# Kernel optimization log

Hardware: AMD Instinct MI355X
Metric: run time of the kernel (lower is better)

The kernel has to match this reference:

```python
import jax, jax.numpy as jnp
import numpy as np
import math

N_POLY = 300
N_DEG = 3
OUT_DIM = 2 * (N_DEG + 1)  # 8 sampled points per query
HEADS = 8


def _grid_sample(x, grid):
    # x: [B,C,H,W], grid: [B,Q,N,2] in [-1,1]; bilinear, zeros padding, align_corners=False
    B, C, H, W = x.shape
    ix = (grid[..., 0] + 1.0) * (W * 0.5) - 0.5
    iy = (grid[..., 1] + 1.0) * (H * 0.5) - 0.5
    ix0 = jnp.floor(ix)
    iy0 = jnp.floor(iy)
    wx1 = ix - ix0
    wy1 = iy - iy0
    x0 = ix0.astype(jnp.int32)
    y0 = iy0.astype(jnp.int32)
    xf = x.reshape(B, C, H * W)

    def gather(yc, xc):
        valid = (xc >= 0) & (xc < W) & (yc >= 0) & (yc < H)
        idx = jnp.clip(yc, 0, H - 1) * W + jnp.clip(xc, 0, W - 1)  # [B,Q,N]
        vals = jax.vmap(lambda m, i: m[:, i])(xf, idx)  # [B,C,Q,N]
        return vals * valid[:, None].astype(x.dtype)

    out = (gather(y0, x0) * ((1 - wy1) * (1 - wx1))[:, None]
           + gather(y0, x0 + 1) * ((1 - wy1) * wx1)[:, None]
           + gather(y0 + 1, x0) * (wy1 * (1 - wx1))[:, None]
           + gather(y0 + 1, x0 + 1) * (wy1 * wx1)[:, None])
    return out  # [B,C,Q,N]


def setup_inputs() -> dict:
    key = jax.random.key(0)
    B, C, H, W = 16, 256, 64, 96
    ks = list(jax.random.split(key, 20))

    def w(k, shape):
        return jax.random.normal(k, shape, jnp.float32) * (1.0 / np.sqrt(shape[0]))

    d = {}
    d['x'] = jax.random.normal(ks[0], (B, C, H, W), jnp.float32)
    d['qs_w1'] = w(ks[1], (C, 2 * C)); d['qs_b1'] = jnp.zeros((2 * C,), jnp.float32)
    d['qs_w2'] = w(ks[2], (2 * C, 1)); d['qs_b2'] = jnp.zeros((1,), jnp.float32)
    d['rp_w1'] = w(ks[3], (C, 2 * C)); d['rp_b1'] = jnp.zeros((2 * C,), jnp.float32)
    d['rp_w2'] = w(ks[4], (2 * C, OUT_DIM * 2)); d['rp_b2'] = jnp.zeros((OUT_DIM * 2,), jnp.float32)
    d['mha_in_w'] = w(ks[5], (C, 3 * C)); d['mha_in_b'] = jnp.zeros((3 * C,), jnp.float32)
    d['mha_out_w'] = w(ks[6], (C, C)); d['mha_out_b'] = jnp.zeros((C,), jnp.float32)
    d['dq_w'] = w(ks[7], (C, C)); d['dq_b'] = jnp.zeros((C,), jnp.float32)
    d['dk_w'] = w(ks[8], (C, C)); d['dk_b'] = jnp.zeros((C,), jnp.float32)
    d['dv_w'] = w(ks[9], (C, C)); d['dv_b'] = jnp.zeros((C,), jnp.float32)
    d['ln1_g'] = jnp.ones((C,), jnp.float32); d['ln1_b'] = jnp.zeros((C,), jnp.float32)
    d['cl_w1'] = w(ks[10], (C, 2 * C)); d['cl_b1'] = jnp.zeros((2 * C,), jnp.float32)
    d['cl_w2'] = w(ks[11], (2 * C, 1)); d['cl_b2'] = jnp.zeros((1,), jnp.float32)
    d['po_w1'] = w(ks[12], (C, 2 * C)); d['po_b1'] = jnp.zeros((2 * C,), jnp.float32)
    d['po_w2'] = w(ks[13], (2 * C, OUT_DIM)); d['po_b2'] = jnp.zeros((OUT_DIM,), jnp.float32)
    return d


def reference(x, qs_w1, qs_b1, qs_w2, qs_b2, rp_w1, rp_b1, rp_w2, rp_b2,
              mha_in_w, mha_in_b, mha_out_w, mha_out_b,
              dq_w, dq_b, dk_w, dk_b, dv_w, dv_b,
              ln1_g, ln1_b, cl_w1, cl_b1, cl_w2, cl_b2,
              po_w1, po_b1, po_w2, po_b2):
    B, C, H, W = x.shape
    dh = C // HEADS
    scale = 1.0 / math.sqrt(dh)

    memory = x.reshape(B, C, H * W).transpose(0, 2, 1)  # [B,HW,C]
    logits = jax.nn.elu(memory @ qs_w1 + qs_b1) @ qs_w2 + qs_b2  # [B,HW,1]
    _, idxs = jax.lax.top_k(logits[..., 0], N_POLY)  # [B,Q]
    querys = jnp.take_along_axis(memory, idxs[..., None], axis=1)  # [B,Q,C]
    rp = jnp.tanh((memory @ rp_w1 + rp_b1) @ rp_w2 + rp_b2)  # [B,HW,2*OUT_DIM]
    ref = jnp.take_along_axis(rp, idxs[..., None], axis=1).reshape(B, N_POLY, OUT_DIM, 2)

    # self-attention (nn.MultiheadAttention, batch_first, 8 heads)
    qkv = querys @ mha_in_w + mha_in_b
    q, k, v = jnp.split(qkv, 3, axis=-1)
    sh = lambda t: t.reshape(B, N_POLY, HEADS, dh).transpose(0, 2, 1, 3)
    q, k, v = sh(q), sh(k), sh(v)
    att = jax.nn.softmax(jnp.einsum('bhqd,bhkd->bhqk', q, k) * scale, axis=-1)
    o = jnp.einsum('bhqk,bhkd->bhqd', att, v).transpose(0, 2, 1, 3).reshape(B, N_POLY, C)
    o = o @ mha_out_w + mha_out_b
    tgt = querys + o  # dropout is identity in eval
    mu = tgt.mean(-1, keepdims=True)
    var = tgt.var(-1, keepdims=True)
    tgt = (tgt - mu) / jnp.sqrt(var + 1e-5) * ln1_g + ln1_b

    # deformable attention
    dq = (tgt @ dq_w + dq_b).reshape(B, N_POLY, 1, HEADS, dh).transpose(0, 1, 3, 2, 4)  # [B,Q,H,1,dh]
    samp = _grid_sample(x, ref)  # [B,C,Q,N]
    sp = samp.transpose(0, 3, 2, 1)  # [B,N,Q,C] (matches torch transpose(1,-1))
    # faithful to torch .view(B,Q,N,H,dh) on the [B,N,Q,C] contiguous tensor: plain reshape
    dk = (sp @ dk_w + dk_b).reshape(B, N_POLY, OUT_DIM, HEADS, dh).transpose(0, 1, 3, 2, 4)  # [B,Q,H,N,dh]
    dv = (sp @ dv_w + dv_b).reshape(B, N_POLY, OUT_DIM, HEADS, dh).transpose(0, 1, 3, 2, 4)
    a = jax.nn.softmax(jnp.einsum('bqhod,bqhnd->bqhon', dq, dk) * scale, axis=-1)
    out2 = jnp.einsum('bqhon,bqhnd->bqhod', a, dv).reshape(B, N_POLY, C)
    tgt = tgt + out2

    poly = jax.nn.silu(tgt @ po_w1 + po_b1) @ po_w2 + po_b2
    cls = jax.nn.sigmoid(jax.nn.elu(tgt @ cl_w1 + cl_b1) @ cl_w2 + cl_b2)[..., 0]
    return poly.reshape(B, N_POLY, 2, N_DEG + 1), cls
```

## Files before the change

kernel.cpp:

```cpp
#include <hip/hip_runtime.h>
#include <hip/hip_bf16.h>
#include <math.h>

typedef __hip_bfloat16 bf16;

#define B_   16
#define C_   256
#define H_   64
#define W_   96
#define HW_  6144
#define Q_   300
#define NH_  8
#define DH_  32
#define HID_ 512
#define QB_  4
#define SCALE_ 0.17677669529663687f

__device__ __forceinline__ float b2f(bf16 v){ return __bfloat162float(v); }
__device__ __forceinline__ bf16 f2b(float v){ return __float2bfloat16(v); }
__device__ __forceinline__ int clampi(int v, int lo, int hi){
  return v < lo ? lo : (v > hi ? hi : v);
}

__global__ __launch_bounds__(256) void xt_k(const float* __restrict__ x,
                                            float* __restrict__ xt){
  int b  = blockIdx.z;
  int c0 = blockIdx.y*64;
  int p0 = blockIdx.x*64;
  __shared__ float t[64][65];
  int tid = threadIdx.x;
  int tr = tid >> 6;
  int tc = tid & 63;
  #pragma unroll
  for (int i=0;i<16;i++){
    int cc = tr + i*4;
    t[cc][tc] = x[((size_t)b*C_ + c0+cc)*HW_ + p0 + tc];
  }
  __syncthreads();
  #pragma unroll
  for (int i=0;i<16;i++){
    int pp = tr + i*4;
    xt[((size_t)b*HW_ + p0+pp)*C_ + c0 + tc] = t[tc][pp];
  }
}

__global__ __launch_bounds__(256) void score_k(const float* __restrict__ x,
    const float* __restrict__ w1, const float* __restrict__ b1,
    const float* __restrict__ w2, const float* __restrict__ b2,
    float* __restrict__ logits){
  int b = blockIdx.y, hw0 = blockIdx.x*64;
  int tid = threadIdx.x;
  int tc = tid & 31;
  int tr = tid >> 5;
  __shared__ float xs[32][68];
  __shared__ float wsl[32][256];
  float (*red)[33] = (float(*)[33])wsl;
  float part[8];
  #pragma unroll
  for (int i=0;i<8;i++) part[i]=0.f;
  for (int pass=0; pass<2; ++pass){
    float acc[8][8];
    #pragma unroll
    for (int i=0;i<8;i++)
      #pragma unroll
      for (int j=0;j<8;j++) acc[i][j]=0.f;
    for (int kt=0; kt<8; ++kt){
      #pragma unroll
      for (int i=0;i<2;i++){
        int e = tid + i*256;
        int rr4 = e & 15, kk = e >> 4;
        *reinterpret_cast<float4*>(&xs[kk][rr4*4]) =
          *reinterpret_cast<const float4*>(&x[(size_t)(b*C_ + kt*32+kk)*HW_ + hw0 + rr4*4]);
      }
      #pragma unroll
      for (int i=0;i<8;i++){
        int e = tid + i*256;
        int jj4 = e & 63, kk = e >> 6;
        *reinterpret_cast<float4*>(&wsl[kk][jj4*4]) =
          *reinterpret_cast<const float4*>(&w1[(size_t)(kt*32+kk)*HID_ + pass*256 + jj4*4]);
      }
      __syncthreads();
      #pragma unroll
      for (int k=0;k<32;k++){
        float4 a0 = *reinterpret_cast<float4*>(&xs[k][tr*8]);
        float4 a1 = *reinterpret_cast<float4*>(&xs[k][tr*8+4]);
        float4 w0 = *reinterpret_cast<float4*>(&wsl[k][tc*4]);
        float4 w4 = *reinterpret_cast<float4*>(&wsl[k][128 + tc*4]);
        float aa[8] = {a0.x,a0.y,a0.z,a0.w,a1.x,a1.y,a1.z,a1.w};
        float ww[8] = {w0.x,w0.y,w0.z,w0.w,w4.x,w4.y,w4.z,w4.w};
        #pragma unroll
        for (int i=0;i<8;i++)
          #pragma unroll
          for (int j=0;j<8;j++)
            acc[i][j] += aa[i]*ww[j];
      }
      __syncthreads();
    }
    #pragma unroll
    for (int j=0;j<8;j++){
      int col = (j < 4) ? (tc*4 + j) : (128 + tc*4 + (j-4));
      int jg = pass*256 + col;
      float bb = b1[jg], w2v = w2[jg];
      #pragma unroll
      for (int i=0;i<8;i++){
        float h = acc[i][j] + bb;
        h = h > 0.f ? h : expm1f(h);
        part[i] += h * w2v;
      }
    }
  }
  #pragma unroll
  for (int i=0;i<8;i++) red[tr*8+i][tc] = part[i];
  __syncthreads();
  if (tid < 64){
    float s = 0.f;
    for (int t=0;t<32;t++) s += red[tid][t];
    logits[(size_t)b*HW_ + hw0 + tid] = s + b2[0];
  }
}

__global__ __launch_bounds__(1024) void topk_k(const float* __restrict__ logits,
                                               int* __restrict__ idxs){
  int b = blockIdx.x, tid = threadIdx.x;
  __shared__ unsigned long long keys[8192];
  for (int i = tid; i < 8192; i += 1024){
    unsigned long long key = 0ull;
    if (i < HW_){
      float v = logits[(size_t)b*HW_ + i];
      unsigned u = __float_as_uint(v);
      unsigned m = (u & 0x80000000u) ? ~u : (u ^ 0x80000000u);
      if (!(v == v)) m = 0u;
      key = ((unsigned long long)m << 32) | (unsigned)(HW_ - 1 - i);
    }
    keys[i] = key;
  }
  __syncthreads();
  for (int k = 2; k <= 8192; k <<= 1){
    for (int j = k >> 1; j >= 1; j >>= 1){
      for (int i = tid; i < 8192; i += 1024){
        int l = i ^ j;
        if (l > i){
          unsigned long long a = keys[i], c = keys[l];
          bool sw = ((i & k) == 0) ? (a < c) : (a > c);
          if (sw){ keys[i] = c; keys[l] = a; }
        }
      }
      __syncthreads();
    }
  }
  if (tid < Q_){
    int idx = HW_ - 1 - (int)(keys[tid] & 0xFFFFFFFFull);
    idxs[b*Q_ + tid] = idx;
  }
}

template<int XT>
__global__ __launch_bounds__(256) void qproj_k(const float* __restrict__ x,
    const float* __restrict__ xt,
    const int* __restrict__ idxs,
    const float* __restrict__ rw1, const float* __restrict__ rb1,
    const float* __restrict__ rw2, const float* __restrict__ rb2,
    const float* __restrict__ mw,  const float* __restrict__ mb,
    float* __restrict__ refs,
    bf16* __restrict__ qarr, bf16* __restrict__ karr, bf16* __restrict__ varr){
  int blk = blockIdx.x;
  int b = blk/(Q_/QB_), q0 = (blk%(Q_/QB_))*QB_;
  int tid = threadIdx.x;
  __shared__ float rowl[QB_][C_];
  __shared__ float hl[QB_][HID_];
  __shared__ float red[16][17];
  int idxv[QB_];
  #pragma unroll
  for (int j=0;j<QB_;j++) idxv[j] = clampi(idxs[b*Q_+q0+j], 0, HW_-1);
  #pragma unroll
  for (int j=0;j<QB_;j++){
    if (XT) rowl[j][tid] = xt[((size_t)b*HW_ + idxv[j])*C_ + tid];
    else    rowl[j][tid] = x[((size_t)b*C_ + tid)*HW_ + idxv[j]];
  }
  __syncthreads();
  float h0[QB_], h1[QB_];
  #pragma unroll
  for (int j=0;j<QB_;j++){ h0[j]=rb1[tid]; h1[j]=rb1[tid+256]; }
  for (int c=0;c<C_;c++){
    float wv0 = rw1[(size_t)c*HID_ + tid];
    float wv1 = rw1[(size_t)c*HID_ + tid + 256];
    #pragma unroll
    for (int j=0;j<QB_;j++){
      float rv = rowl[j][c];
      h0[j] += rv*wv0; h1[j] += rv*wv1;
    }
  }
  #pragma unroll
  for (int j=0;j<QB_;j++){ hl[j][tid]=h0[j]; hl[j][tid+256]=h1[j]; }
  float aq[QB_], ak[QB_], av[QB_];
  #pragma unroll
  for (int j=0;j<QB_;j++){ aq[j]=mb[tid]; ak[j]=mb[tid+256]; av[j]=mb[tid+512]; }
  for (int c=0;c<C_;c++){
    const float* wr = mw + (size_t)c*768;
    float w0 = wr[tid], w1v = wr[tid+256], w2v = wr[tid+512];
    #pragma unroll
    for (int j=0;j<QB_;j++){
      float rv = rowl[j][c];
      aq[j] += rv*w0; ak[j] += rv*w1v; av[j] += rv*w2v;
    }
  }
  int h = tid>>5, d = tid&31;
  #pragma unroll
  for (int j=0;j<QB_;j++){
    size_t o = (((size_t)b*NH_+h)*Q_+(q0+j))*DH_ + d;
    qarr[o]=f2b(aq[j]); karr[o]=f2b(ak[j]); varr[o]=f2b(av[j]);
  }
  __syncthreads();
  int o = tid & 15, seg = tid >> 4;
  for (int j=0;j<QB_;j++){
    float p = 0.f;
    for (int jj=seg*32; jj<seg*32+32; jj++) p += hl[j][jj]*rw2[jj*16+o];
    red[seg][o] = p;
    __syncthreads();
    if (tid < 16){
      float s = 0.f;
      for (int sg=0; sg<16; sg++) s += red[sg][tid];
      refs[((size_t)b*Q_+(q0+j))*16 + tid] = tanhf(s + rb2[tid]);
    }
    __syncthreads();
  }
}

__global__ __launch_bounds__(256) void attn_k(const bf16* __restrict__ qarr,
    const bf16* __restrict__ karr, const bf16* __restrict__ varr,
    bf16* __restrict__ att_o){
  int blk = blockIdx.x; int bh = blk >> 1, half = blk & 1;
  int tid = threadIdx.x, rg = tid >> 5, lane = tid & 31;
  __shared__ bf16 kk[Q_][34];
  __shared__ bf16 vv[Q_][34];
  __shared__ float ps[8][304];
  __shared__ float qsl[8][32];
  const bf16* kb = karr + (size_t)bh*Q_*DH_;
  const bf16* vb = varr + (size_t)bh*Q_*DH_;
  const bf16* qb = qarr + (size_t)bh*Q_*DH_;
  for (int e=tid; e<Q_*DH_; e+=256){
    int k = e >> 5, d = e & 31;
    kk[k][d] = kb[e];
    vv[k][d] = vb[e];
  }
  __syncthreads();
  int b = bh >> 3, h = bh & 7;
  int rbase = half*150;
  for (int p0=0; p0<150; p0+=8){
    int rr = p0 + rg;
    bool act = rr < 150;
    int r = rbase + (act ? rr : 0);
    float qd = act ? b2f(qb[r*DH_ + lane]) : 0.f;
    qsl[rg][lane] = qd;
    __syncthreads();
    float lmax = -1e30f;
    for (int k=lane; k<Q_; k+=32){
      float s = 0.f;
      #pragma unroll
      for (int d=0; d<DH_; d++) s += qsl[rg][d]*b2f(kk[k][d]);
      s *= SCALE_;
      ps[rg][k] = s;
      lmax = fmaxf(lmax, s);
    }
    #pragma unroll
    for (int off=16; off>=1; off>>=1) lmax = fmaxf(lmax, __shfl_xor(lmax, off, 32));
    float lsum = 0.f;
    for (int k=lane; k<Q_; k+=32){
      float e = expf(ps[rg][k] - lmax);
      ps[rg][k] = e;
      lsum += e;
    }
    #pragma unroll
    for (int off=16; off>=1; off>>=1) lsum += __shfl_xor(lsum, off, 32);
    __syncthreads();
    float out = 0.f;
    for (int k=0;k<Q_;k++) out += ps[rg][k]*b2f(vv[k][lane]);
    if (act) att_o[((size_t)b*Q_ + r)*C_ + h*DH_ + lane] = f2b(out / lsum);
    __syncthreads();
  }
}

template<int XT>
__global__ __launch_bounds__(256) void proj_ln_k(const bf16* __restrict__ att_o,
    const float* __restrict__ x, const float* __restrict__ xt,
    const int* __restrict__ idxs,
    const float* __restrict__ ow, const float* __restrict__ ob,
    const float* __restrict__ g,  const float* __restrict__ beta,
    const float* __restrict__ dqw, const float* __restrict__ dqb,
    float* __restrict__ tgt, float* __restrict__ dqv){
  int blk = blockIdx.x, tid = threadIdx.x;
  int b = blk/Q_, qq = blk%Q_;
  __shared__ float ol[C_];
  __shared__ float yl[C_];
  __shared__ float rs[4], rs2[4];
  size_t base = (size_t)blk*C_;
  ol[tid] = b2f(att_o[base+tid]);
  __syncthreads();
  float acc = ob[tid];
  for (int c=0;c<C_;c++) acc += ol[c]*ow[(size_t)c*C_+tid];
  int idx = clampi(idxs[b*Q_+qq], 0, HW_-1);
  float resid;
  if (XT) resid = xt[((size_t)b*HW_ + idx)*C_ + tid];
  else    resid = x[((size_t)b*C_ + tid)*HW_ + idx];
  float t = resid + acc;
  float s = t, s2 = t*t;
  #pragma unroll
  for (int off=32; off>=1; off>>=1){
    s  += __shfl_xor(s,  off, 64);
    s2 += __shfl_xor(s2, off, 64);
  }
  if ((tid&63)==0){ rs[tid>>6]=s; rs2[tid>>6]=s2; }
  __syncthreads();
  float ts=0.f, ts2=0.f;
  #pragma unroll
  for (int w=0;w<4;w++){ ts+=rs[w]; ts2+=rs2[w]; }
  float mu = ts*(1.f/256.f);
  float var = ts2*(1.f/256.f) - mu*mu;
  if (!(var > 0.f)) var = 0.f;
  float y = (t-mu)*rsqrtf(var+1e-5f)*g[tid] + beta[tid];
  tgt[base+tid] = y;
  yl[tid] = y;
  __syncthreads();
  float a2 = dqb[tid];
  for (int c=0;c<C_;c++) a2 += yl[c]*dqw[(size_t)c*C_+tid];
  dqv[base+tid] = a2;
}

template<int XT>
__global__ __launch_bounds__(512) void deform_k(const float* __restrict__ x,
    const float* __restrict__ xt,
    const float* __restrict__ refs, const float* __restrict__ dqv,
    const float* __restrict__ tgt,
    const float* __restrict__ dkw, const float* __restrict__ dkb,
    const float* __restrict__ dvw, const float* __restrict__ dvb,
    const float* __restrict__ pw1, const float* __restrict__ pb1,
    const float* __restrict__ pw2, const float* __restrict__ pb2,
    const float* __restrict__ cw1, const float* __restrict__ cb1,
    const float* __restrict__ cw2, const float* __restrict__ cb2,
    float* __restrict__ out_poly, float* __restrict__ out_cls){
  int blk = blockIdx.x; int b = blk/(Q_/QB_), qg = blk%(Q_/QB_);
  int q0 = qg*QB_;
  int tid = threadIdx.x;
  int col = tid & 255;
  int half = tid >> 8;
  __shared__ float smem_u[32*C_];
  float (*rows_l)[C_]  = (float(*)[C_])smem_u;
  float (*hp)[HID_]    = (float(*)[HID_])smem_u;
  float (*hc)[HID_]    = (float(*)[HID_])(smem_u + QB_*HID_);
  __shared__ float tl[QB_][C_];
  __shared__ float grefs[32][2];
  __shared__ float redp[16][8];
  __shared__ float redc[16];
  if (tid < 64){
    int rloc = tid >> 1, comp = tid & 1;
    int r = qg*32 + rloc;
    int n = r/Q_, q = r - n*Q_;
    grefs[rloc][comp] = refs[(((size_t)b*Q_+q)*8+n)*2 + comp];
  }
  __syncthreads();
  const float* xc  = x  + ((size_t)b*C_ + col)*HW_;
  const float* xbt = xt + (size_t)b*HW_*C_;
  for (int i=0; i<16; ++i){
    int rloc = half*16 + i;
    float gx = grefs[rloc][0];
    float gy = grefs[rloc][1];
    if (!(gx > -2.f && gx < 2.f)) gx = 0.f;
    if (!(gy > -2.f && gy < 2.f)) gy = 0.f;
    float ix = (gx + 1.f)*48.f - 0.5f;
    float iy = (gy + 1.f)*32.f - 0.5f;
    float fx = floorf(ix), fy = floorf(iy);
    int x0 = (int)fx, y0 = (int)fy;
    float wx1 = ix - fx, wy1 = iy - fy;
    float wx0 = 1.f - wx1, wy0 = 1.f - wy1;
    float v = 0.f;
    if (XT){
      if (y0   >= 0 && y0   < H_ && x0   >= 0 && x0   < W_) v += wy0*wx0*xbt[(size_t)(y0*W_+x0)*C_ + col];
      if (y0   >= 0 && y0   < H_ && x0+1 >= 0 && x0+1 < W_) v += wy0*wx1*xbt[(size_t)(y0*W_+x0+1)*C_ + col];
      if (y0+1 >= 0 && y0+1 < H_ && x0   >= 0 && x0   < W_) v += wy1*wx0*xbt[(size_t)((y0+1)*W_+x0)*C_ + col];
      if (y0+1 >= 0 && y0+1 < H_ && x0+1 >= 0 && x0+1 < W_) v += wy1*wx1*xbt[(size_t)((y0+1)*W_+x0+1)*C_ + col];
    } else {
      if (y0   >= 0 && y0   < H_ && x0   >= 0 && x0   < W_) v += wy0*wx0*xc[y0*W_+x0];
      if (y0   >= 0 && y0   < H_ && x0+1 >= 0 && x0+1 < W_) v += wy0*wx1*xc[y0*W_+x0+1];
      if (y0+1 >= 0 && y0+1 < H_ && x0   >= 0 && x0   < W_) v += wy1*wx0*xc[(y0+1)*W_+x0];
      if (y0+1 >= 0 && y0+1 < H_ && x0+1 >= 0 && x0+1 < W_) v += wy1*wx1*xc[(y0+1)*W_+x0+1];
    }
    rows_l[rloc][col] = v;
  }
  __syncthreads();
  float ka[16], va[16];
  float kbb = dkb[col], vbb = dvb[col];
  #pragma unroll
  for (int rr=0; rr<16; ++rr){ ka[rr]=kbb; va[rr]=vbb; }
  for (int c=0; c<C_; c+=4){
    float wk0 = dkw[(size_t)(c+0)*C_+col], wk1 = dkw[(size_t)(c+1)*C_+col];
    float wk2 = dkw[(size_t)(c+2)*C_+col], wk3 = dkw[(size_t)(c+3)*C_+col];
    float wv0 = dvw[(size_t)(c+0)*C_+col], wv1 = dvw[(size_t)(c+1)*C_+col];
    float wv2 = dvw[(size_t)(c+2)*C_+col], wv3 = dvw[(size_t)(c+3)*C_+col];
    #pragma unroll
    for (int rr=0; rr<16; ++rr){
      float4 rv = *reinterpret_cast<float4*>(&rows_l[half*16+rr][c]);
      ka[rr] += rv.x*wk0 + rv.y*wk1 + rv.z*wk2 + rv.w*wk3;
      va[rr] += rv.x*wv0 + rv.y*wv1 + rv.z*wv2 + rv.w*wv3;
    }
  }
  #pragma unroll
  for (int jq=0; jq<2; ++jq){
    int jj = half*2 + jq;
    int q2 = q0 + jj;
    float qd = dqv[((size_t)b*Q_+q2)*C_ + col];
    float s[8];
    #pragma unroll
    for (int n=0;n<8;n++){
      float t_ = qd * ka[jq*8+n];
      #pragma unroll
      for (int off=16; off>=1; off>>=1) t_ += __shfl_xor(t_, off, 32);
      s[n] = t_ * SCALE_;
    }
    float m = s[0];
    #pragma unroll
    for (int n=1;n<8;n++) m = fmaxf(m, s[n]);
    float e[8], sum = 0.f;
    #pragma unroll
    for (int n=0;n<8;n++){ e[n] = expf(s[n]-m); sum += e[n]; }
    float inv = 1.f/sum;
    float out = 0.f;
    #pragma unroll
    for (int n=0;n<8;n++) out += e[n]*inv*va[jq*8+n];
    tl[jj][col] = tgt[((size_t)b*Q_+q2)*C_ + col] + out;
  }
  __syncthreads();
  float a[QB_], cc[QB_];
  #pragma unroll
  for (int jj=0;jj<QB_;jj++){ a[jj]=pb1[tid]; cc[jj]=cb1[tid]; }
  for (int c=0;c<C_;c++){
    float pwA = pw1[(size_t)c*HID_ + tid];
    float cwA = cw1[(size_t)c*HID_ + tid];
    #pragma unroll
    for (int jj=0;jj<QB_;jj++){
      float rv = tl[jj][c];
      a[jj] += rv*pwA; cc[jj] += rv*cwA;
    }
  }
  #pragma unroll
  for (int jj=0;jj<QB_;jj++){
    hp[jj][tid] = a[jj] * (1.f/(1.f+expf(-a[jj])));
    hc[jj][tid] = cc[jj] > 0.f ? cc[jj] : expm1f(cc[jj]);
  }
  __syncthreads();
  for (int jj=0;jj<QB_;jj++){
    if (tid < 128){
      int o = tid & 7, seg = tid >> 3;
      float p = 0.f;
      for (int j=seg*32; j<seg*32+32; j++) p += hp[jj][j]*pw2[j*8+o];
      redp[seg][o] = p;
    } else if (tid < 144){
      int seg = tid - 128;
      float p = 0.f;
      for (int j=seg*32; j<seg*32+32; j++) p += hc[jj][j]*cw2[j];
      redc[seg] = p;
    }
    __syncthreads();
    if (tid < 8){
      float sm = 0.f;
      for (int sg=0; sg<16; sg++) sm += redp[sg][tid];
      out_poly[((size_t)b*Q_+(q0+jj))*8 + tid] = sm + pb2[tid];
    }
    if (tid == 8){
      float sc = 0.f;
      for (int sg=0; sg<16; sg++) sc += redc[sg];
      sc += cb2[0];
      out_cls[b*Q_+(q0+jj)] = 1.f/(1.f+expf(-sc));
    }
    __syncthreads();
  }
}

extern "C" void kernel_launch(void* const* d_in, const int* in_sizes, int n_in,
                              void* d_out, int out_size, void* d_ws, size_t ws_size,
                              hipStream_t stream){
  (void)in_sizes; (void)out_size;
  if (n_in < 29) return;
  const float* x       = (const float*)d_in[0];
  const float* qs_w1   = (const float*)d_in[1];
  const float* qs_b1   = (const float*)d_in[2];
  const float* qs_w2   = (const float*)d_in[3];
  const float* qs_b2   = (const float*)d_in[4];
  const float* rp_w1   = (const float*)d_in[5];
  const float* rp_b1   = (const float*)d_in[6];
  const float* rp_w2   = (const float*)d_in[7];
  const float* rp_b2   = (const float*)d_in[8];
  const float* mha_in_w  = (const float*)d_in[9];
  const float* mha_in_b  = (const float*)d_in[10];
  const float* mha_out_w = (const float*)d_in[11];
  const float* mha_out_b = (const float*)d_in[12];
  const float* dq_w    = (const float*)d_in[13];
  const float* dq_b    = (const float*)d_in[14];
  const float* dk_w    = (const float*)d_in[15];
  const float* dk_b    = (const float*)d_in[16];
  const float* dv_w    = (const float*)d_in[17];
  const float* dv_b    = (const float*)d_in[18];
  const float* ln1_g   = (const float*)d_in[19];
  const float* ln1_b   = (const float*)d_in[20];
  const float* cl_w1   = (const float*)d_in[21];
  const float* cl_b1   = (const float*)d_in[22];
  const float* cl_w2   = (const float*)d_in[23];
  const float* cl_b2   = (const float*)d_in[24];
  const float* po_w1   = (const float*)d_in[25];
  const float* po_b1   = (const float*)d_in[26];
  const float* po_w2   = (const float*)d_in[27];
  const float* po_b2   = (const float*)d_in[28];

  constexpr size_t QKV1     = (size_t)B_*NH_*Q_*DH_;
  constexpr size_t SZ_R1    = 9830400;
  constexpr size_t OFF_IDXS = SZ_R1;
  constexpr size_t OFF_REFS = OFF_IDXS + 19200;
  constexpr size_t OFF_ATTO = OFF_REFS + 307200;
  constexpr size_t WS_NEED  = OFF_ATTO + 2457600;
  constexpr size_t OFF_XT   = WS_NEED;
  constexpr size_t SZ_XT    = (size_t)B_*HW_*C_*sizeof(float);
  constexpr size_t WS_NEED2 = OFF_XT + SZ_XT;
  if (ws_size < WS_NEED) return;
  const bool use_xt = (ws_size >= WS_NEED2);

  char* ws = (char*)d_ws;
  float* logits = (float*)(ws + 0);
  bf16*  qarr   = (bf16*) (ws + 0);
  bf16*  karr   = qarr + QKV1;
  bf16*  varr   = karr + QKV1;
  float* tgt    = (float*)(ws + 0);
  float* dqv    = (float*)(ws + 4915200);
  int*   idxs   = (int*)  (ws + OFF_IDXS);
  float* refs   = (float*)(ws + OFF_REFS);
  bf16*  att_o  = (bf16*) (ws + OFF_ATTO);
  float* xt     = (float*)(ws + OFF_XT);

  float* out_poly = (float*)d_out;
  float* out_cls  = out_poly + B_*Q_*8;

  if (use_xt)
    xt_k<<<dim3(HW_/64, C_/64, B_), 256, 0, stream>>>(x, xt);

  score_k<<<dim3(HW_/64, B_), 256, 0, stream>>>(x, qs_w1, qs_b1, qs_w2, qs_b2, logits);
  topk_k<<<B_, 1024, 0, stream>>>(logits, idxs);

  if (use_xt){
    qproj_k<1><<<B_*(Q_/QB_), 256, 0, stream>>>(x, xt, idxs, rp_w1, rp_b1, rp_w2, rp_b2,
                                                mha_in_w, mha_in_b, refs, qarr, karr, varr);
  } else {
    qproj_k<0><<<B_*(Q_/QB_), 256, 0, stream>>>(x, xt, idxs, rp_w1, rp_b1, rp_w2, rp_b2,
                                                mha_in_w, mha_in_b, refs, qarr, karr, varr);
  }
  attn_k<<<B_*NH_*2, 256, 0, stream>>>(qarr, karr, varr, att_o);
  if (use_xt){
    proj_ln_k<1><<<B_*Q_, 256, 0, stream>>>(att_o, x, xt, idxs, mha_out_w, mha_out_b,
                                            ln1_g, ln1_b, dq_w, dq_b, tgt, dqv);
    deform_k<1><<<B_*(Q_/QB_), 512, 0, stream>>>(x, xt, refs, dqv, tgt,
                                           dk_w, dk_b, dv_w, dv_b,
                                           po_w1, po_b1, po_w2, po_b2,
                                           cl_w1, cl_b1, cl_w2, cl_b2,
                                           out_poly, out_cls);
  } else {
    proj_ln_k<0><<<B_*Q_, 256, 0, stream>>>(att_o, x, xt, idxs, mha_out_w, mha_out_b,
                                            ln1_g, ln1_b, dq_w, dq_b, tgt, dqv);
    deform_k<0><<<B_*(Q_/QB_), 512, 0, stream>>>(x, xt, refs, dqv, tgt,
                                           dk_w, dk_b, dv_w, dv_b,
                                           po_w1, po_b1, po_w2, po_b2,
                                           cl_w1, cl_b1, cl_w2, cl_b2,
                                           out_poly, out_cls);
  }
}
```

Before: 1.274 ms.

## Raise queries per block in qproj and deform kernels to improve weight reuse

qproj_k now handles 6 queries per block instead of 4, so each weight load is reused across more rows. deform_k moves to 1024 threads covering 8 queries (64 sampled rows) per block, with a ceiling grid and tail guards, and splits the poly and cls MLP first layers across thread halves. The output reductions run for all queries in one pass rather than a per-query loop with syncs. The cost is a larger block, more shared memory and register pressure (launch_bounds 1024), and fewer blocks in the grid.

Measured after the change: 1.375 ms. +7.9%, slower.

```diff
diff --git a/kernel.cpp b/kernel.cpp
--- a/kernel.cpp
+++ b/kernel.cpp
@@ -14,6 +14,9 @@
 #define DH_  32
 #define HID_ 512
 #define QB_  4
+#define QPB_ 6
+#define QBD_ 8
+#define NQG_ ((Q_ + QBD_ - 1)/QBD_)
 #define SCALE_ 0.17677669529663687f
 
 __device__ __forceinline__ float b2f(bf16 v){ return __bfloat162float(v); }
@@ -164,55 +167,55 @@
     float* __restrict__ refs,
     bf16* __restrict__ qarr, bf16* __restrict__ karr, bf16* __restrict__ varr){
   int blk = blockIdx.x;
-  int b = blk/(Q_/QB_), q0 = (blk%(Q_/QB_))*QB_;
+  int b = blk/(Q_/QPB_), q0 = (blk%(Q_/QPB_))*QPB_;
   int tid = threadIdx.x;
-  __shared__ float rowl[QB_][C_];
-  __shared__ float hl[QB_][HID_];
+  __shared__ float rowl[QPB_][C_];
+  __shared__ float hl[QPB_][HID_];
   __shared__ float red[16][17];
-  int idxv[QB_];
-  #pragma unroll
-  for (int j=0;j<QB_;j++) idxv[j] = clampi(idxs[b*Q_+q0+j], 0, HW_-1);
-  #pragma unroll
-  for (int j=0;j<QB_;j++){
+  int idxv[QPB_];
+  #pragma unroll
+  for (int j=0;j<QPB_;j++) idxv[j] = clampi(idxs[b*Q_+q0+j], 0, HW_-1);
+  #pragma unroll
+  for (int j=0;j<QPB_;j++){
     if (XT) rowl[j][tid] = xt[((size_t)b*HW_ + idxv[j])*C_ + tid];
     else    rowl[j][tid] = x[((size_t)b*C_ + tid)*HW_ + idxv[j]];
   }
   __syncthreads();
-  float h0[QB_], h1[QB_];
-  #pragma unroll
-  for (int j=0;j<QB_;j++){ h0[j]=rb1[tid]; h1[j]=rb1[tid+256]; }
+  float h0[QPB_], h1[QPB_];
+  #pragma unroll
+  for (int j=0;j<QPB_;j++){ h0[j]=rb1[tid]; h1[j]=rb1[tid+256]; }
   for (int c=0;c<C_;c++){
     float wv0 = rw1[(size_t)c*HID_ + tid];
     float wv1 = rw1[(size_t)c*HID_ + tid + 256];
     #pragma unroll
-    for (int j=0;j<QB_;j++){
+    for (int j=0;j<QPB_;j++){
       float rv = rowl[j][c];
       h0[j] += rv*wv0; h1[j] += rv*wv1;
     }
   }
   #pragma unroll
-  for (int j=0;j<QB_;j++){ hl[j][tid]=h0[j]; hl[j][tid+256]=h1[j]; }
-  float aq[QB_], ak[QB_], av[QB_];
-  #pragma unroll
-  for (int j=0;j<QB_;j++){ aq[j]=mb[tid]; ak[j]=mb[tid+256]; av[j]=mb[tid+512]; }
+  for (int j=0;j<QPB_;j++){ hl[j][tid]=h0[j]; hl[j][tid+256]=h1[j]; }
+  float aq[QPB_], ak[QPB_], av[QPB_];
+  #pragma unroll
+  for (int j=0;j<QPB_;j++){ aq[j]=mb[tid]; ak[j]=mb[tid+256]; av[j]=mb[tid+512]; }
   for (int c=0;c<C_;c++){
     const float* wr = mw + (size_t)c*768;
     float w0 = wr[tid], w1v = wr[tid+256], w2v = wr[tid+512];
     #pragma unroll
-    for (int j=0;j<QB_;j++){
+    for (int j=0;j<QPB_;j++){
       float rv = rowl[j][c];
       aq[j] += rv*w0; ak[j] += rv*w1v; av[j] += rv*w2v;
     }
   }
   int h = tid>>5, d = tid&31;
   #pragma unroll
-  for (int j=0;j<QB_;j++){
+  for (int j=0;j<QPB_;j++){
     size_t o = (((size_t)b*NH_+h)*Q_+(q0+j))*DH_ + d;
     qarr[o]=f2b(aq[j]); karr[o]=f2b(ak[j]); varr[o]=f2b(av[j]);
   }
   __syncthreads();
   int o = tid & 15, seg = tid >> 4;
-  for (int j=0;j<QB_;j++){
+  for (int j=0;j<QPB_;j++){
     float p = 0.f;
     for (int jj=seg*32; jj<seg*32+32; jj++) p += hl[j][jj]*rw2[jj*16+o];
     red[seg][o] = p;
@@ -327,7 +330,7 @@
 }
 
 template<int XT>
-__global__ __launch_bounds__(512) void deform_k(const float* __restrict__ x,
+__global__ __launch_bounds__(1024, 8) void deform_k(const float* __restrict__ x,
     const float* __restrict__ xt,
     const float* __restrict__ refs, const float* __restrict__ dqv,
     const float* __restrict__ tgt,
@@ -338,30 +341,35 @@
     const float* __restrict__ cw1, const float* __restrict__ cb1,
     const float* __restrict__ cw2, const float* __restrict__ cb2,
     float* __restrict__ out_poly, float* __restrict__ out_cls){
-  int blk = blockIdx.x; int b = blk/(Q_/QB_), qg = blk%(Q_/QB_);
-  int q0 = qg*QB_;
+  int blk = blockIdx.x; int b = blk/NQG_, qg = blk%NQG_;
+  int q0 = qg*QBD_;
   int tid = threadIdx.x;
   int col = tid & 255;
-  int half = tid >> 8;
-  __shared__ float smem_u[32*C_];
-  float (*rows_l)[C_]  = (float(*)[C_])smem_u;
-  float (*hp)[HID_]    = (float(*)[HID_])smem_u;
-  float (*hc)[HID_]    = (float(*)[HID_])(smem_u + QB_*HID_);
-  __shared__ float tl[QB_][C_];
-  __shared__ float grefs[32][2];
-  __shared__ float redp[16][8];
-  __shared__ float redc[16];
-  if (tid < 64){
+  int quarter = tid >> 8;
+  __shared__ float smem_u[64*C_];
+  float (*rows_l)[C_] = (float(*)[C_])smem_u;
+  float (*hp)[HID_]   = (float(*)[HID_])smem_u;
+  float (*hc)[HID_]   = (float(*)[HID_])(smem_u + QBD_*HID_);
+  __shared__ float tl_u[QBD_*C_];
+  float (*tl)[C_]      = (float(*)[C_])tl_u;
+  float (*redp)[16][8] = (float(*)[16][8])tl_u;
+  float *redc          = tl_u + QBD_*16*8;
+  __shared__ float grefs[64][2];
+  if (tid < 128){
     int rloc = tid >> 1, comp = tid & 1;
-    int r = qg*32 + rloc;
-    int n = r/Q_, q = r - n*Q_;
-    grefs[rloc][comp] = refs[(((size_t)b*Q_+q)*8+n)*2 + comp];
+    int r = qg*64 + rloc;
+    float gv = 0.f;
+    if (r < Q_*8){
+      int n = r/Q_, q = r - n*Q_;
+      gv = refs[(((size_t)b*Q_+q)*8+n)*2 + comp];
+    }
+    grefs[rloc][comp] = gv;
   }
   __syncthreads();
   const float* xc  = x  + ((size_t)b*C_ + col)*HW_;
   const float* xbt = xt + (size_t)b*HW_*C_;
   for (int i=0; i<16; ++i){
-    int rloc = half*16 + i;
+    int rloc = quarter*16 + i;
     float gx = grefs[rloc][0];
     float gy = grefs[rloc][1];
     if (!(gx > -2.f && gx < 2.f)) gx = 0.f;
@@ -398,16 +406,17 @@
     float wv2 = dvw[(size_t)(c+2)*C_+col], wv3 = dvw[(size_t)(c+3)*C_+col];
     #pragma unroll
     for (int rr=0; rr<16; ++rr){
-      float4 rv = *reinterpret_cast<float4*>(&rows_l[half*16+rr][c]);
+      float4 rv = *reinterpret_cast<float4*>(&rows_l[quarter*16+rr][c]);
       ka[rr] += rv.x*wk0 + rv.y*wk1 + rv.z*wk2 + rv.w*wk3;
       va[rr] += rv.x*wv0 + rv.y*wv1 + rv.z*wv2 + rv.w*wv3;
     }
   }
   #pragma unroll
   for (int jq=0; jq<2; ++jq){
-    int jj = half*2 + jq;
+    int jj = quarter*2 + jq;
     int q2 = q0 + jj;
-    float qd = dqv[((size_t)b*Q_+q2)*C_ + col];
+    int q2c = q2 < Q_ ? q2 : Q_-1;
+    float qd = dqv[((size_t)b*Q_+q2c)*C_ + col];
     float s[8];
     #pragma unroll
     for (int n=0;n<8;n++){
@@ -426,52 +435,63 @@
     float out = 0.f;
     #pragma unroll
     for (int n=0;n<8;n++) out += e[n]*inv*va[jq*8+n];
-    tl[jj][col] = tgt[((size_t)b*Q_+q2)*C_ + col] + out;
-  }
-  __syncthreads();
-  float a[QB_], cc[QB_];
-  #pragma unroll
-  for (int jj=0;jj<QB_;jj++){ a[jj]=pb1[tid]; cc[jj]=cb1[tid]; }
-  for (int c=0;c<C_;c++){
-    float pwA = pw1[(size_t)c*HID_ + tid];
-    float cwA = cw1[(size_t)c*HID_ + tid];
-    #pragma unroll
-    for (int jj=0;jj<QB_;jj++){
-      float rv = tl[jj][c];
-      a[jj] += rv*pwA; cc[jj] += rv*cwA;
-    }
-  }
-  #pragma unroll
-  for (int jj=0;jj<QB_;jj++){
-    hp[jj][tid] = a[jj] * (1.f/(1.f+expf(-a[jj])));
-    hc[jj][tid] = cc[jj] > 0.f ? cc[jj] : expm1f(cc[jj]);
-  }
-  __syncthreads();
-  for (int jj=0;jj<QB_;jj++){
+    tl[jj][col] = tgt[((size_t)b*Q_+q2c)*C_ + col] + out;
+  }
+  __syncthreads();
+  {
+    int unit = tid & 511;
+    const float* wmat = (tid < 512) ? pw1 : cw1;
+    float bias = (tid < 512) ? pb1[unit] : cb1[unit];
+    float acc8[QBD_];
+    #pragma unroll
+    for (int jj=0;jj<QBD_;jj++) acc8[jj] = bias;
+    for (int c=0;c<C_;c++){
+      float wv = wmat[(size_t)c*HID_ + unit];
+      #pragma unroll
+      for (int jj=0;jj<QBD_;jj++) acc8[jj] += tl[jj][c]*wv;
+    }
+    if (tid < 512){
+      #pragma unroll
+      for (int jj=0;jj<QBD_;jj++)
+        hp[jj][unit] = acc8[jj] * (1.f/(1.f+expf(-acc8[jj])));
+    } else {
+      #pragma unroll
+      for (int jj=0;jj<QBD_;jj++)
+        hc[jj][unit] = acc8[jj] > 0.f ? acc8[jj] : expm1f(acc8[jj]);
+    }
+  }
+  __syncthreads();
+  {
+    int jj = tid >> 7, t2 = tid & 127;
+    int seg = t2 >> 3, o = t2 & 7;
+    float p = 0.f;
+    for (int j=seg*32; j<seg*32+32; j++) p += hp[jj][j]*pw2[j*8+o];
+    redp[jj][seg][o] = p;
     if (tid < 128){
-      int o = tid & 7, seg = tid >> 3;
-      float p = 0.f;
-      for (int j=seg*32; j<seg*32+32; j++) p += hp[jj][j]*pw2[j*8+o];
-      redp[seg][o] = p;
-    } else if (tid < 144){
-      int seg = tid - 128;
-      float p = 0.f;
-      for (int j=seg*32; j<seg*32+32; j++) p += hc[jj][j]*cw2[j];
-      redc[seg] = p;
-    }
-    __syncthreads();
-    if (tid < 8){
+      int jc = tid >> 4, sc = tid & 15;
+      float p2 = 0.f;
+      for (int j=sc*32; j<sc*32+32; j++) p2 += hc[jc][j]*cw2[j];
+      redc[jc*16+sc] = p2;
+    }
+  }
+  __syncthreads();
+  if (tid < 64){
+    int jj = tid >> 3, o = tid & 7;
+    int q2 = q0 + jj;
+    if (q2 < Q_){
       float sm = 0.f;
-      for (int sg=0; sg<16; sg++) sm += redp[sg][tid];
-      out_poly[((size_t)b*Q_+(q0+jj))*8 + tid] = sm + pb2[tid];
-    }
-    if (tid == 8){
+      for (int sg=0; sg<16; sg++) sm += redp[jj][sg][o];
+      out_poly[((size_t)b*Q_+q2)*8 + o] = sm + pb2[o];
+    }
+  } else if (tid < 72){
+    int jj = tid - 64;
+    int q2 = q0 + jj;
+    if (q2 < Q_){
       float sc = 0.f;
-      for (int sg=0; sg<16; sg++) sc += redc[sg];
+      for (int sg=0; sg<16; sg++) sc += redc[jj*16+sg];
       sc += cb2[0];
-      out_cls[b*Q_+(q0+jj)] = 1.f/(1.f+expf(-sc));
-    }
-    __syncthreads();
+      out_cls[b*Q_+q2] = 1.f/(1.f+expf(-sc));
+    }
   }
 }
 
@@ -544,17 +564,17 @@
   topk_k<<<B_, 1024, 0, stream>>>(logits, idxs);
 
   if (use_xt){
-    qproj_k<1><<<B_*(Q_/QB_), 256, 0, stream>>>(x, xt, idxs, rp_w1, rp_b1, rp_w2, rp_b2,
-                                                mha_in_w, mha_in_b, refs, qarr, karr, varr);
+    qproj_k<1><<<B_*(Q_/QPB_), 256, 0, stream>>>(x, xt, idxs, rp_w1, rp_b1, rp_w2, rp_b2,
+                                                 mha_in_w, mha_in_b, refs, qarr, karr, varr);
   } else {
-    qproj_k<0><<<B_*(Q_/QB_), 256, 0, stream>>>(x, xt, idxs, rp_w1, rp_b1, rp_w2, rp_b2,
-                                                mha_in_w, mha_in_b, refs, qarr, karr, varr);
+    qproj_k<0><<<B_*(Q_/QPB_), 256, 0, stream>>>(x, xt, idxs, rp_w1, rp_b1, rp_w2, rp_b2,
+                                                 mha_in_w, mha_in_b, refs, qarr, karr, varr);
   }
   attn_k<<<B_*NH_*2, 256, 0, stream>>>(qarr, karr, varr, att_o);
   if (use_xt){
     proj_ln_k<1><<<B_*Q_, 256, 0, stream>>>(att_o, x, xt, idxs, mha_out_w, mha_out_b,
                                             ln1_g, ln1_b, dq_w, dq_b, tgt, dqv);
-    deform_k<1><<<B_*(Q_/QB_), 512, 0, stream>>>(x, xt, refs, dqv, tgt,
+    deform_k<1><<<B_*NQG_, 1024, 0, stream>>>(x, xt, refs, dqv, tgt,
                                            dk_w, dk_b, dv_w, dv_b,
                                            po_w1, po_b1, po_w2, po_b2,
                                            cl_w1, cl_b1, cl_w2, cl_b2,
@@ -562,7 +582,7 @@
   } else {
     proj_ln_k<0><<<B_*Q_, 256, 0, stream>>>(att_o, x, xt, idxs, mha_out_w, mha_out_b,
                                             ln1_g, ln1_b, dq_w, dq_b, tgt, dqv);
-    deform_k<0><<<B_*(Q_/QB_), 512, 0, stream>>>(x, xt, refs, dqv, tgt,
+    deform_k<0><<<B_*NQG_, 1024, 0, stream>>>(x, xt, refs, dqv, tgt,
                                            dk_w, dk_b, dv_w, dv_b,
                                            po_w1, po_b1, po_w2, po_b2,
                                            cl_w1, cl_b1, cl_w2, cl_b2,
```
